# Kernel tuning notes

Measured on AMD Instinct MI355X. Metric: run time of the kernel, lower is better.

## Reference

```python
import jax, jax.numpy as jnp
import numpy as np

N = 100000
E = 1600000
IN, HID, OUT, HEADS = 256, 16, 64, 8
NEG_SLOPE = 0.2


def gat_conv(x, src, dst, W, att_s, att_d, bias, heads, out_c, concat):
    n = x.shape[0]
    h = (x @ W).reshape(n, heads, out_c)              # [N,H,C]
    a_s = jnp.einsum('nhc,hc->nh', h, att_s)          # [N,H]
    a_d = jnp.einsum('nhc,hc->nh', h, att_d)          # [N,H]
    logits = jax.nn.leaky_relu(a_s[src] + a_d[dst], NEG_SLOPE)  # [E,H]
    m = jax.ops.segment_max(logits, dst, num_segments=n)        # [N,H]
    m = jnp.where(jnp.isfinite(m), m, 0.0)
    e = jnp.exp(logits - m[dst])                                 # [E,H]
    denom = jax.ops.segment_sum(e, dst, num_segments=n)         # [N,H]
    alpha = e / (denom[dst] + 1e-16)                             # [E,H]
    msg = h[src] * alpha[:, :, None]                             # [E,H,C]
    out = jax.ops.segment_sum(msg, dst, num_segments=n)          # [N,H,C]
    out = out.reshape(n, heads * out_c) if concat else out.mean(axis=1)
    return out + bias


def setup_inputs() -> dict:
    key = jax.random.key(0)
    ks = jax.random.split(key, 10)
    g = lambda k, shp, fan: jax.random.normal(k, shp, jnp.float32) * np.sqrt(2.0 / fan)
    x = jax.random.normal(ks[0], (N, IN), jnp.float32)
    edge_index = jax.random.randint(ks[1], (2, E), 0, N, jnp.int32)
    W1 = g(ks[2], (IN, HEADS * HID), IN)
    att1_s = g(ks[3], (HEADS, HID), HID)
    att1_d = g(ks[4], (HEADS, HID), HID)
    b1 = jnp.zeros((HEADS * HID,), jnp.float32)
    W2 = g(ks[5], (HEADS * HID, OUT), HEADS * HID)
    att2_s = g(ks[6], (1, OUT), OUT)
    att2_d = g(ks[7], (1, OUT), OUT)
    b2 = jnp.zeros((OUT,), jnp.float32)
    return {"x": x, "edge_index": edge_index, "W1": W1, "att1_s": att1_s,
            "att1_d": att1_d, "b1": b1, "W2": W2, "att2_s": att2_s,
            "att2_d": att2_d, "b2": b2}


def reference(x, edge_index, W1, att1_s, att1_d, b1, W2, att2_s, att2_d, b2):
    src, dst = edge_index[0], edge_index[1]
    h = gat_conv(x, src, dst, W1, att1_s, att1_d, b1, HEADS, HID, True)
    h = jax.nn.elu(h)  # dropout = identity in eval mode
    h = gat_conv(h, src, dst, W2, att2_s, att2_d, b2, 1, OUT, False)
    return jax.nn.log_softmax(h, axis=1)
```

## Files before the change

### kernel.cpp

```cpp
#include <hip/hip_runtime.h>
#include <math.h>

#define N_NODES 100000
#define N_EDGES 1600000
#define GEMM1_BLOCKS ((N_NODES + 63) / 64)
#define FUSED_BLOCKS (GEMM1_BLOCKS * 5)
#define KCHAIN 24

typedef __attribute__((ext_vector_type(8))) short short8;
typedef __attribute__((ext_vector_type(4))) float floatx4;

__device__ __forceinline__ float lrelu(float v) {
    return (v > 0.f) ? v : 0.2f * v;
}

__device__ __forceinline__ unsigned short f2bf(float f) {
    unsigned int u = __float_as_uint(f);
    u += 0x7fff + ((u >> 16) & 1);
    return (unsigned short)(u >> 16);
}

__device__ __forceinline__ float bflo(unsigned int u) { return __uint_as_float(u << 16); }
__device__ __forceinline__ float bfhi(unsigned int u) { return __uint_as_float(u & 0xffff0000u); }

__global__ void prep_kernel(const float* __restrict__ W1, const float* __restrict__ W2,
                            unsigned short* __restrict__ w1b, unsigned short* __restrict__ w2b) {
    int idx = blockIdx.x * 256 + threadIdx.x;
    if (idx < 4096) {
        int lane = idx & 63;
        int ts = idx >> 6;
        int t = ts >> 3, ks = ts & 7;
        int quad = lane >> 4, l15 = lane & 15;
        int kbase = ks * 32 + quad * 8;
        unsigned short o[8];
        #pragma unroll
        for (int j = 0; j < 8; j++)
            o[j] = f2bf(W1[(size_t)(kbase + j) * 128 + t * 16 + l15]);
        uint4 pk;
        pk.x = o[0] | ((unsigned int)o[1] << 16);
        pk.y = o[2] | ((unsigned int)o[3] << 16);
        pk.z = o[4] | ((unsigned int)o[5] << 16);
        pk.w = o[6] | ((unsigned int)o[7] << 16);
        ((uint4*)w1b)[idx] = pk;
    } else if (idx < 4096 + 1024) {
        int idx2 = idx - 4096;
        int lane = idx2 & 63;
        int ts = idx2 >> 6;
        int t = ts >> 2, ks = ts & 3;
        int quad = lane >> 4, l15 = lane & 15;
        int kbase = ks * 32 + quad * 8;
        unsigned short o[8];
        #pragma unroll
        for (int j = 0; j < 8; j++)
            o[j] = f2bf(W2[(size_t)(kbase + j) * 64 + t * 16 + l15]);
        uint4 pk;
        pk.x = o[0] | ((unsigned int)o[1] << 16);
        pk.y = o[2] | ((unsigned int)o[3] << 16);
        pk.z = o[4] | ((unsigned int)o[5] << 16);
        pk.w = o[6] | ((unsigned int)o[7] << 16);
        ((uint4*)w2b)[idx2] = pk;
    }
}

__global__ void __launch_bounds__(256) gemm1_link_kernel(
        const float* __restrict__ x, const short8* __restrict__ w1b,
        const float* __restrict__ att_s, const float* __restrict__ att_d,
        unsigned short* __restrict__ h1b, float* __restrict__ a1s, float* __restrict__ a1d,
        const int* __restrict__ ei, int* __restrict__ head, int2* __restrict__ rec8) {
    const int bid = blockIdx.x;
    if (bid % 5 != 0) {
        int lid = bid - bid / 5 - 1;
        int e = lid * 256 + threadIdx.x;
        if (e < N_EDGES) {
            int s = ei[e];
            int d = ei[N_EDGES + e];
            int old = atomicExch(&head[d], e);
            rec8[e] = make_int2(old, s);
        }
        return;
    }
    const int gid = bid / 5;
    const int lane = threadIdx.x & 63;
    const int wv = threadIdx.x >> 6;
    const int quad = lane >> 4;
    const int l15 = lane & 15;
    const int M = N_NODES;

    const int rowA = gid * 64 + wv * 16 + l15;
    const bool rowAok = rowA < M;
    const float4* xrow4 = (const float4*)(x + (size_t)rowA * 256);

    floatx4 acc[8];
    #pragma unroll
    for (int t = 0; t < 8; t++) acc[t] = (floatx4){0.f, 0.f, 0.f, 0.f};

    #pragma unroll
    for (int ks = 0; ks < 8; ks++) {
        float4 p0, p1;
        if (rowAok) {
            p0 = xrow4[ks * 8 + quad * 2];
            p1 = xrow4[ks * 8 + quad * 2 + 1];
        } else {
            p0 = make_float4(0.f, 0.f, 0.f, 0.f);
            p1 = p0;
        }
        short8 af;
        af[0] = (short)f2bf(p0.x); af[1] = (short)f2bf(p0.y);
        af[2] = (short)f2bf(p0.z); af[3] = (short)f2bf(p0.w);
        af[4] = (short)f2bf(p1.x); af[5] = (short)f2bf(p1.y);
        af[6] = (short)f2bf(p1.z); af[7] = (short)f2bf(p1.w);
        #pragma unroll
        for (int t = 0; t < 8; t++) {
            short8 bf = w1b[(t * 8 + ks) * 64 + lane];
            acc[t] = __builtin_amdgcn_mfma_f32_16x16x32_bf16(af, bf, acc[t], 0, 0, 0);
        }
    }

    const int rowC0 = gid * 64 + wv * 16 + quad * 4;
    #pragma unroll
    for (int t = 0; t < 8; t++) {
        float asw = att_s[t * 16 + l15];
        float adw = att_d[t * 16 + l15];
        #pragma unroll
        for (int r = 0; r < 4; r++) {
            int grow = rowC0 + r;
            float c = acc[t][r];
            if (grow < M) h1b[(size_t)grow * 128 + t * 16 + l15] = f2bf(c);
            float ps = c * asw;
            float pd = c * adw;
            ps += __shfl_xor(ps, 1, 64); ps += __shfl_xor(ps, 2, 64);
            ps += __shfl_xor(ps, 4, 64); ps += __shfl_xor(ps, 8, 64);
            pd += __shfl_xor(pd, 1, 64); pd += __shfl_xor(pd, 2, 64);
            pd += __shfl_xor(pd, 4, 64); pd += __shfl_xor(pd, 8, 64);
            if (l15 == 0 && grow < M) { a1s[grow * 8 + t] = ps; a1d[grow * 8 + t] = pd; }
        }
    }
}

__global__ void __launch_bounds__(256) csr_build_kernel(
        const int* __restrict__ head, const int2* __restrict__ rec8,
        int* __restrict__ rowstart, int* __restrict__ deg,
        int* __restrict__ counter, int* __restrict__ csr_src, int n) {
    int i = blockIdx.x * 256 + threadIdx.x;
    int lane = threadIdx.x & 63;
    int e = (i < n) ? head[i] : -1;
    int srcbuf[KCHAIN];
    int c = 0;
    #pragma unroll
    for (int k = 0; k < KCHAIN; k++) {
        srcbuf[k] = 0;
        if (e >= 0) {
            int2 r = rec8[e];
            srcbuf[k] = r.y;
            e = r.x;
            c++;
        }
    }
    int etail = e;
    while (e >= 0) {
        e = ((const int*)rec8)[(size_t)e * 2];
        c++;
    }
    int pre = c;
    #pragma unroll
    for (int off = 1; off < 64; off <<= 1) {
        int v = __shfl_up(pre, off, 64);
        if (lane >= off) pre += v;
    }
    int total = __shfl(pre, 63, 64);
    int base = 0;
    if (lane == 63) base = atomicAdd(counter, total);
    base = __shfl(base, 63, 64);
    if (i < n) {
        int rs = base + pre - c;
        rowstart[i] = rs;
        deg[i] = c;
        #pragma unroll
        for (int k = 0; k < KCHAIN; k++)
            if (k < c) csr_src[rs + k] = srcbuf[k];
        e = etail;
        int idx = rs + KCHAIN;
        while (e >= 0) {
            int2 r = rec8[e];
            csr_src[idx++] = r.y;
            e = r.x;
        }
    }
}

__global__ void __launch_bounds__(256) agg1_kernel(
        const unsigned short* __restrict__ h1b, const float* __restrict__ a1s,
        const float* __restrict__ a1d, const int* __restrict__ rowstart,
        const int* __restrict__ deg, const int* __restrict__ csr_src,
        const float* __restrict__ b1, unsigned int* __restrict__ h2b, int n) {
    const int lane = threadIdx.x & 63;
    const int node = blockIdx.x * 4 + (threadIdx.x >> 6);
    if (node >= n) return;
    const int h = lane >> 3;
    const int start = rowstart[node];
    const int d = deg[node];
    const float ad = a1d[node * 8 + h];
    float l = 0.f, acc0 = 0.f, acc1 = 0.f;
    int i = 0;
    for (; i + 8 <= d; i += 8) {
        int s[8];
        float as[8];
        unsigned int u[8];
        #pragma unroll
        for (int k = 0; k < 8; k++) s[k] = csr_src[start + i + k];
        #pragma unroll
        for (int k = 0; k < 8; k++) as[k] = a1s[s[k] * 8 + h];
        #pragma unroll
        for (int k = 0; k < 8; k++)
            u[k] = *(const unsigned int*)(h1b + (size_t)s[k] * 128 + lane * 2);
        #pragma unroll
        for (int k = 0; k < 8; k++) {
            float e = __expf(lrelu(as[k] + ad));
            l += e;
            acc0 += e * bflo(u[k]);
            acc1 += e * bfhi(u[k]);
        }
    }
    for (; i + 4 <= d; i += 4) {
        int s[4];
        float as[4];
        unsigned int u[4];
        #pragma unroll
        for (int k = 0; k < 4; k++) s[k] = csr_src[start + i + k];
        #pragma unroll
        for (int k = 0; k < 4; k++) as[k] = a1s[s[k] * 8 + h];
        #pragma unroll
        for (int k = 0; k < 4; k++)
            u[k] = *(const unsigned int*)(h1b + (size_t)s[k] * 128 + lane * 2);
        #pragma unroll
        for (int k = 0; k < 4; k++) {
            float e = __expf(lrelu(as[k] + ad));
            l += e;
            acc0 += e * bflo(u[k]);
            acc1 += e * bfhi(u[k]);
        }
    }
    for (; i < d; i++) {
        int s0 = csr_src[start + i];
        float as0 = a1s[s0 * 8 + h];
        unsigned int u0 = *(const unsigned int*)(h1b + (size_t)s0 * 128 + lane * 2);
        float e0 = __expf(lrelu(as0 + ad));
        l += e0;
        acc0 += e0 * bflo(u0);
        acc1 += e0 * bfhi(u0);
    }
    float inv = 1.f / (l + 1e-16f);
    float v0 = acc0 * inv + b1[lane * 2];
    float v1 = acc1 * inv + b1[lane * 2 + 1];
    v0 = (v0 > 0.f) ? v0 : expm1f(v0);
    v1 = (v1 > 0.f) ? v1 : expm1f(v1);
    h2b[(size_t)node * 64 + lane] = (unsigned int)f2bf(v0) | ((unsigned int)f2bf(v1) << 16);
}

__global__ void __launch_bounds__(256) gemm2_kernel(
        const short8* __restrict__ h2f, const short8* __restrict__ w2b,
        const float* __restrict__ att_s, const float* __restrict__ att_d,
        unsigned short* __restrict__ t2b, float* __restrict__ a2s, float* __restrict__ a2d,
        int n) {
    const int lane = threadIdx.x & 63;
    const int wv = threadIdx.x >> 6;
    const int quad = lane >> 4;
    const int l15 = lane & 15;

    const int rowA = blockIdx.x * 64 + wv * 16 + l15;
    const bool rowAok = rowA < n;

    floatx4 acc[4];
    #pragma unroll
    for (int t = 0; t < 4; t++) acc[t] = (floatx4){0.f, 0.f, 0.f, 0.f};

    #pragma unroll
    for (int ks = 0; ks < 4; ks++) {
        short8 af = {0, 0, 0, 0, 0, 0, 0, 0};
        if (rowAok) af = h2f[(size_t)rowA * 16 + ks * 4 + quad];
        #pragma unroll
        for (int t = 0; t < 4; t++) {
            short8 bf = w2b[(t * 4 + ks) * 64 + lane];
            acc[t] = __builtin_amdgcn_mfma_f32_16x16x32_bf16(af, bf, acc[t], 0, 0, 0);
        }
    }

    const int rowC0 = blockIdx.x * 64 + wv * 16 + quad * 4;
    float asw[4], adw[4];
    #pragma unroll
    for (int t = 0; t < 4; t++) {
        asw[t] = att_s[t * 16 + l15];
        adw[t] = att_d[t * 16 + l15];
    }
    #pragma unroll
    for (int r = 0; r < 4; r++) {
        int grow = rowC0 + r;
        bool ok = grow < n;
        float ps = 0.f, pd = 0.f;
        #pragma unroll
        for (int t = 0; t < 4; t++) {
            float c = acc[t][r];
            if (ok) t2b[(size_t)grow * 64 + t * 16 + l15] = f2bf(c);
            ps += c * asw[t];
            pd += c * adw[t];
        }
        ps += __shfl_xor(ps, 1, 64); ps += __shfl_xor(ps, 2, 64);
        ps += __shfl_xor(ps, 4, 64); ps += __shfl_xor(ps, 8, 64);
        pd += __shfl_xor(pd, 1, 64); pd += __shfl_xor(pd, 2, 64);
        pd += __shfl_xor(pd, 4, 64); pd += __shfl_xor(pd, 8, 64);
        if (l15 == 0 && ok) { a2s[grow] = ps; a2d[grow] = pd; }
    }
}

__global__ void __launch_bounds__(256) agg2_kernel(
        const unsigned short* __restrict__ t2b, const float* __restrict__ a2s,
        const float* __restrict__ a2d, const int* __restrict__ rowstart,
        const int* __restrict__ deg, const int* __restrict__ csr_src,
        const float* __restrict__ b2, float* __restrict__ out, int n) {
    const int lane = threadIdx.x & 63;
    const int node = blockIdx.x * 4 + (threadIdx.x >> 6);
    if (node >= n) return;
    const int start = rowstart[node];
    const int d = deg[node];
    const float ad = a2d[node];
    float l = 0.f, acc = 0.f;
    int i = 0;
    for (; i + 8 <= d; i += 8) {
        int s[8];
        float as[8];
        unsigned short u[8];
        #pragma unroll
        for (int k = 0; k < 8; k++) s[k] = csr_src[start + i + k];
        #pragma unroll
        for (int k = 0; k < 8; k++) as[k] = a2s[s[k]];
        #pragma unroll
        for (int k = 0; k < 8; k++) u[k] = t2b[(size_t)s[k] * 64 + lane];
        #pragma unroll
        for (int k = 0; k < 8; k++) {
            float e = __expf(lrelu(as[k] + ad));
            l += e;
            acc += e * __uint_as_float(((unsigned int)u[k]) << 16);
        }
    }
    for (; i + 4 <= d; i += 4) {
        int s[4];
        float as[4];
        unsigned short u[4];
        #pragma unroll
        for (int k = 0; k < 4; k++) s[k] = csr_src[start + i + k];
        #pragma unroll
        for (int k = 0; k < 4; k++) as[k] = a2s[s[k]];
        #pragma unroll
        for (int k = 0; k < 4; k++) u[k] = t2b[(size_t)s[k] * 64 + lane];
        #pragma unroll
        for (int k = 0; k < 4; k++) {
            float e = __expf(lrelu(as[k] + ad));
            l += e;
            acc += e * __uint_as_float(((unsigned int)u[k]) << 16);
        }
    }
    for (; i < d; i++) {
        int s0 = csr_src[start + i];
        float as0 = a2s[s0];
        unsigned short u0 = t2b[(size_t)s0 * 64 + lane];
        float e0 = __expf(lrelu(as0 + ad));
        l += e0;
        acc += e0 * __uint_as_float(((unsigned int)u0) << 16);
    }
    float v = acc / (l + 1e-16f) + b2[lane];
    float mx = v;
    #pragma unroll
    for (int off = 32; off >= 1; off >>= 1) mx = fmaxf(mx, __shfl_xor(mx, off, 64));
    float ex = expf(v - mx);
    float s2 = ex;
    #pragma unroll
    for (int off = 32; off >= 1; off >>= 1) s2 += __shfl_xor(s2, off, 64);
    out[(size_t)node * 64 + lane] = v - mx - logf(s2);
}


extern "C" void kernel_launch(void* const* d_in, const int* in_sizes, int n_in,
                              void* d_out, int out_size, void* d_ws, size_t ws_size,
                              hipStream_t stream) {
    const float* x     = (const float*)d_in[0];
    const int*   ei    = (const int*)d_in[1];
    const float* W1    = (const float*)d_in[2];
    const float* att1s = (const float*)d_in[3];
    const float* att1d = (const float*)d_in[4];
    const float* b1    = (const float*)d_in[5];
    const float* W2    = (const float*)d_in[6];
    const float* att2s = (const float*)d_in[7];
    const float* att2d = (const float*)d_in[8];
    const float* b2    = (const float*)d_in[9];
    float* out = (float*)d_out;

    const int N = N_NODES, E = N_EDGES;

    char* p = (char*)d_ws;
    auto take = [&](size_t bytes) {
        char* r = p;
        p += (bytes + 255) & ~(size_t)255;
        return (void*)r;
    };
    int*            head     = (int*)take((size_t)N * 4);
    int*            deg      = (int*)take((size_t)N * 4);
    int*            rowstart = (int*)take((size_t)N * 4);
    int*            counter  = (int*)take(256);
    int2*           rec8     = (int2*)take((size_t)E * 8);
    int*            csr_src  = (int*)take((size_t)E * 4);
    unsigned short* w1b      = (unsigned short*)take(64 * 64 * 16);
    unsigned short* w2b      = (unsigned short*)take(16 * 64 * 16);
    unsigned short* h1b      = (unsigned short*)take((size_t)N * 128 * 2);
    float*          a1s      = (float*)take((size_t)N * 8 * 4);
    float*          a1d      = (float*)take((size_t)N * 8 * 4);
    unsigned int*   h2b      = (unsigned int*)take((size_t)N * 64 * 4);
    unsigned short* t2b      = (unsigned short*)take((size_t)N * 64 * 2);
    float* a2s = a1s;
    float* a2d = a1d;

    hipMemsetAsync(head, 0xFF, (size_t)N * 4, stream);
    hipMemsetAsync(counter, 0, 4, stream);

    prep_kernel<<<20, 256, 0, stream>>>(W1, W2, w1b, w2b);
    gemm1_link_kernel<<<FUSED_BLOCKS, 256, 0, stream>>>(
        x, (const short8*)w1b, att1s, att1d, h1b, a1s, a1d, ei, head, rec8);
    csr_build_kernel<<<(N + 255) / 256, 256, 0, stream>>>(head, rec8, rowstart, deg,
                                                          counter, csr_src, N);
    agg1_kernel<<<(N + 3) / 4, 256, 0, stream>>>(h1b, a1s, a1d, rowstart, deg, csr_src,
                                                 b1, h2b, N);
    gemm2_kernel<<<(N + 63) / 64, 256, 0, stream>>>((const short8*)h2b, (const short8*)w2b,
                                                    att2s, att2d, t2b, a2s, a2d, N);
    agg2_kernel<<<(N + 3) / 4, 256, 0, stream>>>(t2b, a2s, a2d, rowstart, deg, csr_src,
                                                 b2, out, N);
}
```

Baseline: 443.8 us.

## Replace linked-list CSR build with two-level bucket partition sort

Replaces the per-destination linked list, built with atomicExch and walked pointer by pointer, with a counting-sort CSR build. A histogram over 512-node buckets, a scan, and a partition pass pack source and low destination bits into one word. A per-bucket kernel then does a local histogram, scan and scatter in shared memory. This removes long dependent pointer-chasing chains and random 8-byte record reads, but adds four kernel launches and drops the overlap with the first GEMM that the fused gemm1_link kernel provided.

```diff
diff --git a/kernel.cpp b/kernel.cpp
--- a/kernel.cpp
+++ b/kernel.cpp
@@ -4,8 +4,8 @@
 #define N_NODES 100000
 #define N_EDGES 1600000
 #define GEMM1_BLOCKS ((N_NODES + 63) / 64)
-#define FUSED_BLOCKS (GEMM1_BLOCKS * 5)
-#define KCHAIN 24
+#define NBKT 196
+#define PART_BLOCKS ((N_EDGES + 4095) / 4096)
 
 typedef __attribute__((ext_vector_type(8))) short short8;
 typedef __attribute__((ext_vector_type(4))) float floatx4;
@@ -22,6 +22,7 @@
 
 __device__ __forceinline__ float bflo(unsigned int u) { return __uint_as_float(u << 16); }
 __device__ __forceinline__ float bfhi(unsigned int u) { return __uint_as_float(u & 0xffff0000u); }
+__device__ __forceinline__ float bfs(unsigned short s) { return __uint_as_float(((unsigned int)s) << 16); }
 
 __global__ void prep_kernel(const float* __restrict__ W1, const float* __restrict__ W2,
                             unsigned short* __restrict__ w1b, unsigned short* __restrict__ w2b) {
@@ -62,24 +63,125 @@
     }
 }
 
-__global__ void __launch_bounds__(256) gemm1_link_kernel(
-        const float* __restrict__ x, const short8* __restrict__ w1b,
-        const float* __restrict__ att_s, const float* __restrict__ att_d,
-        unsigned short* __restrict__ h1b, float* __restrict__ a1s, float* __restrict__ a1d,
-        const int* __restrict__ ei, int* __restrict__ head, int2* __restrict__ rec8) {
-    const int bid = blockIdx.x;
-    if (bid % 5 != 0) {
-        int lid = bid - bid / 5 - 1;
-        int e = lid * 256 + threadIdx.x;
+__global__ void __launch_bounds__(256) hist_kernel(const int* __restrict__ ei,
+                                                   int* __restrict__ bkt_count) {
+    __shared__ int h[NBKT];
+    for (int i = threadIdx.x; i < NBKT; i += 256) h[i] = 0;
+    __syncthreads();
+    int base = blockIdx.x * 4096;
+    #pragma unroll
+    for (int it = 0; it < 16; it++) {
+        int e = base + it * 256 + (int)threadIdx.x;
+        if (e < N_EDGES) atomicAdd(&h[ei[N_EDGES + e] >> 9], 1);
+    }
+    __syncthreads();
+    for (int i = threadIdx.x; i < NBKT; i += 256)
+        if (h[i]) atomicAdd(&bkt_count[i], h[i]);
+}
+
+__global__ void scan_kernel(const int* __restrict__ bkt_count, int* __restrict__ bkt_base,
+                            int* __restrict__ bkt_cursor) {
+    __shared__ int ps[256];
+    int tid = threadIdx.x;
+    int v = (tid < NBKT) ? bkt_count[tid] : 0;
+    ps[tid] = v;
+    __syncthreads();
+    for (int off = 1; off < 256; off <<= 1) {
+        int t = (tid >= off) ? ps[tid - off] : 0;
+        __syncthreads();
+        ps[tid] += t;
+        __syncthreads();
+    }
+    int excl = (tid > 0) ? ps[tid - 1] : 0;
+    if (tid < NBKT) { bkt_base[tid] = excl; bkt_cursor[tid] = excl; }
+    if (tid == NBKT) bkt_base[NBKT] = N_EDGES;
+}
+
+__global__ void __launch_bounds__(256) part_kernel(const int* __restrict__ ei,
+                                                   int* __restrict__ bkt_cursor,
+                                                   int* __restrict__ ebuf) {
+    __shared__ int lcnt[NBKT];
+    __shared__ int lbase[NBKT];
+    for (int i = threadIdx.x; i < NBKT; i += 256) lcnt[i] = 0;
+    __syncthreads();
+    int base = blockIdx.x * 4096;
+    int pk[16], bb[16];
+    #pragma unroll
+    for (int it = 0; it < 16; it++) {
+        int e = base + it * 256 + (int)threadIdx.x;
+        bb[it] = -1;
+        pk[it] = 0;
         if (e < N_EDGES) {
             int s = ei[e];
             int d = ei[N_EDGES + e];
-            int old = atomicExch(&head[d], e);
-            rec8[e] = make_int2(old, s);
-        }
-        return;
-    }
-    const int gid = bid / 5;
+            bb[it] = d >> 9;
+            pk[it] = s | ((d & 511) << 17);
+            atomicAdd(&lcnt[bb[it]], 1);
+        }
+    }
+    __syncthreads();
+    for (int i = threadIdx.x; i < NBKT; i += 256) {
+        int c = lcnt[i];
+        lbase[i] = c ? atomicAdd(&bkt_cursor[i], c) : 0;
+        lcnt[i] = 0;
+    }
+    __syncthreads();
+    #pragma unroll
+    for (int it = 0; it < 16; it++) {
+        if (bb[it] >= 0) {
+            int off = atomicAdd(&lcnt[bb[it]], 1);
+            ebuf[lbase[bb[it]] + off] = pk[it];
+        }
+    }
+}
+
+__global__ void __launch_bounds__(256) csr2_kernel(const int* __restrict__ ebuf,
+                                                   const int* __restrict__ bkt_base,
+                                                   int* __restrict__ rowstart,
+                                                   int* __restrict__ deg,
+                                                   int* __restrict__ csr_src) {
+    __shared__ int h[512];
+    __shared__ int cur[512];
+    __shared__ int ps[256];
+    const int b = blockIdx.x;
+    const int s = bkt_base[b];
+    const int e = bkt_base[b + 1];
+    const int tid = threadIdx.x;
+    h[tid] = 0;
+    h[tid + 256] = 0;
+    __syncthreads();
+    for (int i = s + tid; i < e; i += 256)
+        atomicAdd(&h[((unsigned)ebuf[i]) >> 17], 1);
+    __syncthreads();
+    int a0 = h[2 * tid], a1 = h[2 * tid + 1];
+    ps[tid] = a0 + a1;
+    __syncthreads();
+    for (int off = 1; off < 256; off <<= 1) {
+        int t = (tid >= off) ? ps[tid - off] : 0;
+        __syncthreads();
+        ps[tid] += t;
+        __syncthreads();
+    }
+    int pbase = (tid > 0) ? ps[tid - 1] : 0;
+    int n0 = b * 512 + 2 * tid;
+    int n1 = n0 + 1;
+    cur[2 * tid] = s + pbase;
+    cur[2 * tid + 1] = s + pbase + a0;
+    if (n0 < N_NODES) { rowstart[n0] = s + pbase; deg[n0] = a0; }
+    if (n1 < N_NODES) { rowstart[n1] = s + pbase + a0; deg[n1] = a1; }
+    __syncthreads();
+    for (int i = s + tid; i < e; i += 256) {
+        unsigned pkv = (unsigned)ebuf[i];
+        int pos = atomicAdd(&cur[pkv >> 17], 1);
+        csr_src[pos] = pkv & 0x1FFFF;
+    }
+}
+
+__global__ void __launch_bounds__(256) gemm1_kernel(
+        const float* __restrict__ x, const short8* __restrict__ w1b,
+        const float* __restrict__ att_s, const float* __restrict__ att_d,
+        unsigned short* __restrict__ h1b, float* __restrict__ a1s, float* __restrict__ a1d) {
+    const int gid = blockIdx.x;
     const int lane = threadIdx.x & 63;
     const int wv = threadIdx.x >> 6;
     const int quad = lane >> 4;
@@ -133,57 +235,6 @@
             pd += __shfl_xor(pd, 1, 64); pd += __shfl_xor(pd, 2, 64);
             pd += __shfl_xor(pd, 4, 64); pd += __shfl_xor(pd, 8, 64);
             if (l15 == 0 && grow < M) { a1s[grow * 8 + t] = ps; a1d[grow * 8 + t] = pd; }
-        }
-    }
-}
-
-__global__ void __launch_bounds__(256) csr_build_kernel(
-        const int* __restrict__ head, const int2* __restrict__ rec8,
-        int* __restrict__ rowstart, int* __restrict__ deg,
-        int* __restrict__ counter, int* __restrict__ csr_src, int n) {
-    int i = blockIdx.x * 256 + threadIdx.x;
-    int lane = threadIdx.x & 63;
-    int e = (i < n) ? head[i] : -1;
-    int srcbuf[KCHAIN];
-    int c = 0;
-    #pragma unroll
-    for (int k = 0; k < KCHAIN; k++) {
-        srcbuf[k] = 0;
-        if (e >= 0) {
-            int2 r = rec8[e];
-            srcbuf[k] = r.y;
-            e = r.x;
-            c++;
-        }
-    }
-    int etail = e;
-    while (e >= 0) {
-        e = ((const int*)rec8)[(size_t)e * 2];
-        c++;
-    }
-    int pre = c;
-    #pragma unroll
-    for (int off = 1; off < 64; off <<= 1) {
-        int v = __shfl_up(pre, off, 64);
-        if (lane >= off) pre += v;
-    }
-    int total = __shfl(pre, 63, 64);
-    int base = 0;
-    if (lane == 63) base = atomicAdd(counter, total);
-    base = __shfl(base, 63, 64);
-    if (i < n) {
-        int rs = base + pre - c;
-        rowstart[i] = rs;
-        deg[i] = c;
-        #pragma unroll
-        for (int k = 0; k < KCHAIN; k++)
-            if (k < c) csr_src[rs + k] = srcbuf[k];
-        e = etail;
-        int idx = rs + KCHAIN;
-        while (e >= 0) {
-            int2 r = rec8[e];
-            csr_src[idx++] = r.y;
-            e = r.x;
         }
     }
 }
@@ -339,7 +390,7 @@
         for (int k = 0; k < 8; k++) {
             float e = __expf(lrelu(as[k] + ad));
             l += e;
-            acc += e * __uint_as_float(((unsigned int)u[k]) << 16);
+            acc += e * bfs(u[k]);
         }
     }
     for (; i + 4 <= d; i += 4) {
@@ -356,7 +407,7 @@
         for (int k = 0; k < 4; k++) {
             float e = __expf(lrelu(as[k] + ad));
             l += e;
-            acc += e * __uint_as_float(((unsigned int)u[k]) << 16);
+            acc += e * bfs(u[k]);
         }
     }
     for (; i < d; i++) {
@@ -365,7 +416,7 @@
         unsigned short u0 = t2b[(size_t)s0 * 64 + lane];
         float e0 = __expf(lrelu(as0 + ad));
         l += e0;
-        acc += e0 * __uint_as_float(((unsigned int)u0) << 16);
+        acc += e0 * bfs(u0);
     }
     float v = acc / (l + 1e-16f) + b2[lane];
     float mx = v;
@@ -402,30 +453,32 @@
         p += (bytes + 255) & ~(size_t)255;
         return (void*)r;
     };
-    int*            head     = (int*)take((size_t)N * 4);
-    int*            deg      = (int*)take((size_t)N * 4);
-    int*            rowstart = (int*)take((size_t)N * 4);
-    int*            counter  = (int*)take(256);
-    int2*           rec8     = (int2*)take((size_t)E * 8);
-    int*            csr_src  = (int*)take((size_t)E * 4);
-    unsigned short* w1b      = (unsigned short*)take(64 * 64 * 16);
-    unsigned short* w2b      = (unsigned short*)take(16 * 64 * 16);
-    unsigned short* h1b      = (unsigned short*)take((size_t)N * 128 * 2);
-    float*          a1s      = (float*)take((size_t)N * 8 * 4);
-    float*          a1d      = (float*)take((size_t)N * 8 * 4);
-    unsigned int*   h2b      = (unsigned int*)take((size_t)N * 64 * 4);
-    unsigned short* t2b      = (unsigned short*)take((size_t)N * 64 * 2);
+    int*            bkt_count  = (int*)take(256 * 4);
+    int*            bkt_base   = (int*)take(257 * 4);
+    int*            bkt_cursor = (int*)take(256 * 4);
+    int*            ebuf       = (int*)take((size_t)E * 4);
+    int*            deg        = (int*)take((size_t)N * 4);
+    int*            rowstart   = (int*)take((size_t)N * 4);
+    int*            csr_src    = (int*)take((size_t)E * 4);
+    unsigned short* w1b        = (unsigned short*)take(64 * 64 * 16);
+    unsigned short* w2b        = (unsigned short*)take(16 * 64 * 16);
+    unsigned short* h1b        = (unsigned short*)take((size_t)N * 128 * 2);
+    float*          a1s        = (float*)take((size_t)N * 8 * 4);
+    float*          a1d        = (float*)take((size_t)N * 8 * 4);
+    unsigned int*   h2b        = (unsigned int*)take((size_t)N * 64 * 4);
+    unsigned short* t2b        = (unsigned short*)take((size_t)N * 64 * 2);
     float* a2s = a1s;
     float* a2d = a1d;
 
-    hipMemsetAsync(head, 0xFF, (size_t)N * 4, stream);
-    hipMemsetAsync(counter, 0, 4, stream);
+    hipMemsetAsync(bkt_count, 0, 256 * 4, stream);
 
     prep_kernel<<<20, 256, 0, stream>>>(W1, W2, w1b, w2b);
-    gemm1_link_kernel<<<FUSED_BLOCKS, 256, 0, stream>>>(
-        x, (const short8*)w1b, att1s, att1d, h1b, a1s, a1d, ei, head, rec8);
-    csr_build_kernel<<<(N + 255) / 256, 256, 0, stream>>>(head, rec8, rowstart, deg,
-                                                          counter, csr_src, N);
+    hist_kernel<<<PART_BLOCKS, 256, 0, stream>>>(ei, bkt_count);
+    scan_kernel<<<1, 256, 0, stream>>>(bkt_count, bkt_base, bkt_cursor);
+    part_kernel<<<PART_BLOCKS, 256, 0, stream>>>(ei, bkt_cursor, ebuf);
+    csr2_kernel<<<NBKT, 256, 0, stream>>>(ebuf, bkt_base, rowstart, deg, csr_src);
+    gemm1_kernel<<<GEMM1_BLOCKS, 256, 0, stream>>>(
+        x, (const short8*)w1b, att1s, att1d, h1b, a1s, a1d);
     agg1_kernel<<<(N + 3) / 4, 256, 0, stream>>>(h1b, a1s, a1d, rowstart, deg, csr_src,
                                                  b1, h2b, N);
     gemm2_kernel<<<(N + 63) / 64, 256, 0, stream>>>((const short8*)h2b, (const short8*)w2b,
```

New measurement: 428.5 us. 3.4% less time.
